# Kernel optimization log

Hardware: AMD Instinct MI355X
Metric: run time of the kernel (lower is better)

The kernel has to match this reference:

```python
import jax, jax.numpy as jnp
import numpy as np

B, S, D, H, HD, L, E, K, M, V = 1, 2048, 1024, 16, 64, 2, 8, 2, 768, 32000
EPS = 1e-06
THETA = 1000000.0


def rmsnorm(x, w, eps=EPS):
    xf = x.astype(jnp.float32)
    var = jnp.mean(xf * xf, axis=-1, keepdims=True)
    return (w * (xf * jax.lax.rsqrt(var + eps))).astype(x.dtype)


def apply_rope(x, cos, sin):
    # x: [B,S,H,HD], cos/sin: [S,HD]; rotate_half convention (HF Qwen3)
    c = cos[None, :, None, :]
    s = sin[None, :, None, :]
    x1, x2 = jnp.split(x, 2, axis=-1)
    rot = jnp.concatenate([-x2, x1], axis=-1)
    return x * c + rot * s


def setup_inputs() -> dict:
    key = jax.random.key(0)
    ks = jax.random.split(key, 16)
    std = 0.02
    inp = {}
    inp['input_ids'] = jax.random.randint(ks[0], (B, S), 0, V)
    inp['embed'] = jax.random.normal(ks[1], (V, D), jnp.float32) * std
    inp['wq'] = jax.random.normal(ks[2], (L, D, H * HD), jnp.float32) * std
    inp['wk'] = jax.random.normal(ks[3], (L, D, H * HD), jnp.float32) * std
    inp['wv'] = jax.random.normal(ks[4], (L, D, H * HD), jnp.float32) * std
    inp['wo'] = jax.random.normal(ks[5], (L, H * HD, D), jnp.float32) * std
    inp['q_norm_w'] = jnp.ones((L, HD), jnp.float32)
    inp['k_norm_w'] = jnp.ones((L, HD), jnp.float32)
    inp['attn_norm_w'] = jnp.ones((L, D), jnp.float32)
    inp['ffn_norm_w'] = jnp.ones((L, D), jnp.float32)
    inp['gate_w'] = jax.random.normal(ks[6], (L, D, E), jnp.float32) * std
    inp['w_gate'] = jax.random.normal(ks[7], (L, E, D, M), jnp.float32) * std
    inp['w_up'] = jax.random.normal(ks[8], (L, E, D, M), jnp.float32) * std
    inp['w_down'] = jax.random.normal(ks[9], (L, E, M, D), jnp.float32) * std
    inp['final_norm_w'] = jnp.ones((D,), jnp.float32)
    inp['out_w'] = jax.random.normal(ks[10], (D, V), jnp.float32) * (D ** -0.5)
    # rope cache: cos/sin with duplicated freqs (HF default rope)
    inv_freq = 1.0 / (THETA ** (jnp.arange(0, HD, 2, dtype=jnp.float32) / HD))
    freqs = jnp.outer(jnp.arange(S, dtype=jnp.float32), inv_freq)  # [S,HD/2]
    emb = jnp.concatenate([freqs, freqs], axis=-1)  # [S,HD]
    inp['cos'] = jnp.cos(emb)
    inp['sin'] = jnp.sin(emb)
    return inp


def reference(input_ids, embed, wq, wk, wv, wo, q_norm_w, k_norm_w, attn_norm_w,
              ffn_norm_w, gate_w, w_gate, w_up, w_down, final_norm_w, out_w, cos, sin):
    h = embed[input_ids]  # [B,S,D]
    causal = jnp.tril(jnp.ones((S, S), bool))[None, None]  # [1,1,S,S]
    scale = 1.0 / np.sqrt(HD)

    def layer(h, p):
        Wq, Wk, Wv, Wo, qn, kn, an, fn, gw, Wg, Wu, Wd = p
        # --- attention ---
        x = rmsnorm(h, an)
        q = (x @ Wq).reshape(B, S, H, HD)
        k = (x @ Wk).reshape(B, S, H, HD)
        v = (x @ Wv).reshape(B, S, H, HD)
        q = apply_rope(rmsnorm(q, qn), cos, sin)
        k = apply_rope(rmsnorm(k, kn), cos, sin)
        scores = jnp.einsum('bqhd,bkhd->bhqk', q, k) * scale
        scores = jnp.where(causal, scores, jnp.finfo(scores.dtype).min)
        attn = jax.nn.softmax(scores, axis=-1)
        o = jnp.einsum('bhqk,bkhd->bqhd', attn, v).reshape(B, S, H * HD) @ Wo
        h = h + o
        # --- sparse MoE ---
        x = rmsnorm(h, fn).reshape(-1, D)  # [T,D]
        probs = jax.nn.softmax((x @ gw).astype(jnp.float32), axis=-1)  # [T,E]
        vals, idx = jax.lax.top_k(probs, K)
        vals = vals / jnp.sum(vals, axis=-1, keepdims=True)  # norm_topk_prob=True
        T = x.shape[0]
        dense = jnp.zeros((T, E), x.dtype).at[jnp.arange(T)[:, None], idx].set(vals.astype(x.dtype))
        g = jnp.einsum('td,edm->tem', x, Wg)
        u = jnp.einsum('td,edm->tem', x, Wu)
        y = jnp.einsum('tem,emd->ted', jax.nn.silu(g) * u, Wd)
        moe = jnp.einsum('te,ted->td', dense, y).reshape(B, S, D)
        return h + moe, None

    h, _ = jax.lax.scan(layer, h, (wq, wk, wv, wo, q_norm_w, k_norm_w, attn_norm_w,
                                   ffn_norm_w, gate_w, w_gate, w_up, w_down))
    h = rmsnorm(h, final_norm_w)
    return h @ out_w  # [B,S,V]
```

## Files before the change

### kernel.cpp

```cpp
#include <hip/hip_runtime.h>
#include <hip/hip_bf16.h>


constexpr int S_ = 2048, D_ = 1024, H_ = 16, HD_ = 64, E_ = 8, MF_ = 768, V_ = 32000;

typedef short  short8 __attribute__((ext_vector_type(8)));
typedef float  f32x4  __attribute__((ext_vector_type(4)));

static __device__ __forceinline__ unsigned short f2bf(float f) {
    unsigned u = __float_as_uint(f);
    u += 0x7FFF + ((u >> 16) & 1);
    return (unsigned short)(u >> 16);
}

__global__ __launch_bounds__(256) void k_gather(const int* __restrict__ ids,
                                                const float* __restrict__ emb,
                                                float* __restrict__ h) {
    int tok = blockIdx.x;
    int id  = ids[tok];
    const float4* src = (const float4*)(emb + (long)id * D_);
    float4*       dst = (float4*)(h + (long)tok * D_);
    dst[threadIdx.x] = src[threadIdx.x];
}

template <int BF>
__global__ __launch_bounds__(256) void k_rmsnorm(const float* __restrict__ in,
                                                 const float* __restrict__ w,
                                                 float* __restrict__ outf,
                                                 unsigned short* __restrict__ outb) {
    int row = blockIdx.x, t = threadIdx.x;
    float4 x = ((const float4*)(in + (long)row * D_))[t];
    float ss = x.x * x.x + x.y * x.y + x.z * x.z + x.w * x.w;
#pragma unroll
    for (int m = 32; m >= 1; m >>= 1) ss += __shfl_xor(ss, m);
    __shared__ float ps[4];
    if ((t & 63) == 0) ps[t >> 6] = ss;
    __syncthreads();
    float tot   = ps[0] + ps[1] + ps[2] + ps[3];
    float scale = 1.0f / sqrtf(tot * (1.0f / D_) + 1e-6f);
    float4 wv = ((const float4*)w)[t];
    float4 o;
    o.x = x.x * scale * wv.x; o.y = x.y * scale * wv.y;
    o.z = x.z * scale * wv.z; o.w = x.w * scale * wv.w;
    if (BF) {
        ushort4 ub;
        ub.x = f2bf(o.x); ub.y = f2bf(o.y); ub.z = f2bf(o.z); ub.w = f2bf(o.w);
        *(ushort4*)(outb + (long)row * D_ + t * 4) = ub;
    } else {
        ((float4*)(outf + (long)row * D_))[t] = o;
    }
}

__global__ __launch_bounds__(256) void k_qkrope(float* __restrict__ q, float* __restrict__ k,
                                                const float* __restrict__ qn,
                                                const float* __restrict__ kn,
                                                const float* __restrict__ cosb,
                                                const float* __restrict__ sinb) {
    int wid  = (blockIdx.x << 2) | (threadIdx.x >> 6);
    int lane = threadIdx.x & 63;
    int tensor = wid >> 15;
    int rem    = wid & 32767;
    int tok = rem >> 4, head = rem & 15;
    float* ptr = tensor ? k : q;
    const float* nw = tensor ? kn : qn;
    long off = ((long)tok * H_ + head) * HD_ + lane;
    float v = ptr[off];
    float ss = v * v;
#pragma unroll
    for (int m = 32; m >= 1; m >>= 1) ss += __shfl_xor(ss, m);
    float xn = v * (1.0f / sqrtf(ss * (1.0f / HD_) + 1e-6f)) * nw[lane];
    float other = __shfl_xor(xn, 32);
    float rot = (lane < 32) ? -other : other;
    ptr[off] = xn * cosb[tok * HD_ + lane] + rot * sinb[tok * HD_ + lane];
}

static __device__ __forceinline__ void splitpack2(float x0, float x1,
                                                  unsigned& wh, unsigned& wm,
                                                  unsigned& wl) {
    unsigned u0 = __float_as_uint(x0), u1 = __float_as_uint(x1);
    unsigned h0 = u0 & 0xFFFF0000u,    h1 = u1 & 0xFFFF0000u;
    float r0 = x0 - __uint_as_float(h0), r1 = x1 - __uint_as_float(h1);
    unsigned m0 = __float_as_uint(r0) & 0xFFFF0000u;
    unsigned m1 = __float_as_uint(r1) & 0xFFFF0000u;
    float s0 = r0 - __uint_as_float(m0), s1 = r1 - __uint_as_float(m1);
    unsigned l0 = __float_as_uint(s0),   l1 = __float_as_uint(s1);
    wh = (h0 >> 16) | h1;
    wm = (m0 >> 16) | m1;
    wl = (l0 >> 16) | (l1 & 0xFFFF0000u);
}

static __device__ __forceinline__ void split8(const float* v,
                                              uint4& qh, uint4& qm, uint4& ql) {
    unsigned ph[4], pm[4], pl[4];
#pragma unroll
    for (int j = 0; j < 4; j++) splitpack2(v[2 * j], v[2 * j + 1], ph[j], pm[j], pl[j]);
    qh = make_uint4(ph[0], ph[1], ph[2], ph[3]);
    qm = make_uint4(pm[0], pm[1], pm[2], pm[3]);
    ql = make_uint4(pl[0], pl[1], pl[2], pl[3]);
}

template <int IND, int EPI>
__global__ __launch_bounds__(256) void k_gemm_s6(const float* __restrict__ A,
                                                 const float* __restrict__ B0,
                                                 const float* __restrict__ B1,
                                                 const float* __restrict__ B2,
                                                 float* __restrict__ C,
                                                 const int* __restrict__ offs,
                                                 const int* __restrict__ rows,
                                                 const float* __restrict__ rwgt,
                                                 float* __restrict__ hout,
                                                 int Mtot, int N, int K,
                                                 long bStrideZ, long cStrideZ) {
    int z = blockIdx.z;
    int ms, me;
    if (offs) { ms = offs[z]; me = offs[z + 1]; }
    else      { ms = 0; me = Mtot; }
    int p0 = ms + blockIdx.y * 128;
    if (p0 >= me) return;
    const float* Bz;
    if (B1) Bz = (z == 0) ? B0 : (z == 1) ? B1 : B2;
    else    Bz = B0 + (long)z * bStrideZ;
    float* Cz = C ? (C + (long)z * cStrideZ) : nullptr;
    int n0 = blockIdx.x * 128;

    __shared__ __align__(16) unsigned short As[3][128][40];
    __shared__ __align__(16) unsigned short Bs[3][128][40];

    int t = threadIdx.x;
    int lane = t & 63, wave = t >> 6;
    int wm = (wave >> 1) * 64, wn = (wave & 1) * 64;
    int ln = lane & 15, lq = lane >> 4;

    f32x4 acc[4][4];
    f32x4 zero4 = {0.f, 0.f, 0.f, 0.f};
#pragma unroll
    for (int r = 0; r < 4; r++)
#pragma unroll
        for (int c = 0; c < 4; c++) acc[r][c] = zero4;

    int arow = t >> 1, ak0 = (t & 1) * 16;
    const float* aptr = nullptr;
    {
        int pA = p0 + arow;
        if (pA < me) {
            int srow = IND ? rows[pA] : pA;
            aptr = A + (long)srow * K + ak0;
        }
    }
    int brow = t >> 1, bk0 = (t & 1) * 16;
    const float* bbase = Bz + (n0 + brow);

    for (int k0 = 0; k0 < K; k0 += 32) {
        float va[16];
        if (aptr) {
#pragma unroll
            for (int c4 = 0; c4 < 4; c4++) {
                float4 f = *(const float4*)(aptr + k0 + c4 * 4);
                va[c4 * 4 + 0] = f.x; va[c4 * 4 + 1] = f.y;
                va[c4 * 4 + 2] = f.z; va[c4 * 4 + 3] = f.w;
            }
        } else {
#pragma unroll
            for (int j = 0; j < 16; j++) va[j] = 0.f;
        }
        uint4 ah0, am0, al0, ah1, am1, al1;
        split8(va,     ah0, am0, al0);
        split8(va + 8, ah1, am1, al1);
        float vb[16];
        {
            const float* bp = bbase + (long)(k0 + bk0) * N;
#pragma unroll
            for (int j = 0; j < 16; j++) vb[j] = bp[(long)j * N];
        }
        uint4 bh0, bm0, bl0, bh1, bm1, bl1;
        split8(vb,     bh0, bm0, bl0);
        split8(vb + 8, bh1, bm1, bl1);

        __syncthreads();
        *(uint4*)&As[0][arow][ak0]     = ah0;
        *(uint4*)&As[0][arow][ak0 + 8] = ah1;
        *(uint4*)&As[1][arow][ak0]     = am0;
        *(uint4*)&As[1][arow][ak0 + 8] = am1;
        *(uint4*)&As[2][arow][ak0]     = al0;
        *(uint4*)&As[2][arow][ak0 + 8] = al1;
        *(uint4*)&Bs[0][brow][bk0]     = bh0;
        *(uint4*)&Bs[0][brow][bk0 + 8] = bh1;
        *(uint4*)&Bs[1][brow][bk0]     = bm0;
        *(uint4*)&Bs[1][brow][bk0 + 8] = bm1;
        *(uint4*)&Bs[2][brow][bk0]     = bl0;
        *(uint4*)&Bs[2][brow][bk0 + 8] = bl1;
        __syncthreads();

        short8 fah[4], fam[4], fal[4];
#pragma unroll
        for (int r = 0; r < 4; r++) {
            fah[r] = *(const short8*)&As[0][wm + 16 * r + ln][lq * 8];
            fam[r] = *(const short8*)&As[1][wm + 16 * r + ln][lq * 8];
            fal[r] = *(const short8*)&As[2][wm + 16 * r + ln][lq * 8];
        }
#pragma unroll
        for (int c = 0; c < 4; c++) {
            short8 fbh = *(const short8*)&Bs[0][wn + 16 * c + ln][lq * 8];
            short8 fbm = *(const short8*)&Bs[1][wn + 16 * c + ln][lq * 8];
            short8 fbl = *(const short8*)&Bs[2][wn + 16 * c + ln][lq * 8];
#pragma unroll
            for (int r = 0; r < 4; r++) {
                f32x4 a2 = acc[r][c];
                a2 = __builtin_amdgcn_mfma_f32_16x16x32_bf16(fah[r], fbh, a2, 0, 0, 0);
                a2 = __builtin_amdgcn_mfma_f32_16x16x32_bf16(fah[r], fbm, a2, 0, 0, 0);
                a2 = __builtin_amdgcn_mfma_f32_16x16x32_bf16(fam[r], fbh, a2, 0, 0, 0);
                a2 = __builtin_amdgcn_mfma_f32_16x16x32_bf16(fah[r], fbl, a2, 0, 0, 0);
                a2 = __builtin_amdgcn_mfma_f32_16x16x32_bf16(fam[r], fbm, a2, 0, 0, 0);
                a2 = __builtin_amdgcn_mfma_f32_16x16x32_bf16(fal[r], fbh, a2, 0, 0, 0);
                acc[r][c] = a2;
            }
        }
    }

#pragma unroll
    for (int r = 0; r < 4; r++)
#pragma unroll
        for (int c = 0; c < 4; c++) {
            int rowb = wm + 16 * r + lq * 4;
            int col  = n0 + wn + 16 * c + ln;
#pragma unroll
            for (int i = 0; i < 4; i++) {
                int p = p0 + rowb + i;
                if (p >= me) continue;
                if (EPI == 2) {
                    atomicAdd(hout + (long)rows[p] * N + col, rwgt[p] * acc[r][c][i]);
                } else if (EPI == 1) {
                    float* cp = Cz + (long)p * N + col;
                    *cp += acc[r][c][i];
                } else {
                    Cz[(long)p * N + col] = acc[r][c][i];
                }
            }
        }
}

__global__ __launch_bounds__(256) void k_attn(const float* __restrict__ q,
                                              const float* __restrict__ k,
                                              const float* __restrict__ v,
                                              float* __restrict__ o) {
    int head = blockIdx.y;
    int q0   = blockIdx.x * 32;
    __shared__ __align__(16) float Qs[32][68];
    __shared__ __align__(16) float Kt[64][68];
    __shared__ __align__(16) float Vs[64][68];
    __shared__ __align__(16) float Ss[32][68];
    __shared__ float red[32][8];
    __shared__ float mrow[32], lrow[32], arow[32];
    int t = threadIdx.x;
    int r = t >> 3, c0 = (t & 7) * 8;
    float o8[8] = {0.f, 0.f, 0.f, 0.f, 0.f, 0.f, 0.f, 0.f};
    {
        int qr = t >> 3, d0 = (t & 7) * 8;
        const float* qp = q + ((long)(q0 + qr) * H_ + head) * HD_ + d0;
        *(float4*)&Qs[qr][d0]     = *(const float4*)qp;
        *(float4*)&Qs[qr][d0 + 4] = *(const float4*)(qp + 4);
    }
    if (t < 32) { mrow[t] = -3.402823466e38f; lrow[t] = 0.f; }
    int ktmax = (q0 + 31) >> 6;
    for (int kt = 0; kt <= ktmax; kt++) {
        __syncthreads();
        {
            int row = t >> 2, d0 = (t & 3) * 16;
            const float* kp = k + ((long)(kt * 64 + row) * H_ + head) * HD_ + d0;
            const float* vp = v + ((long)(kt * 64 + row) * H_ + head) * HD_ + d0;
#pragma unroll
            for (int j = 0; j < 4; j++) {
                float4 kv = *(const float4*)(kp + 4 * j);
                float4 vv = *(const float4*)(vp + 4 * j);
                *(float4*)&Vs[row][d0 + 4 * j] = vv;
                Kt[d0 + 4 * j + 0][row] = kv.x;
                Kt[d0 + 4 * j + 1][row] = kv.y;
                Kt[d0 + 4 * j + 2][row] = kv.z;
                Kt[d0 + 4 * j + 3][row] = kv.w;
            }
        }
        __syncthreads();
        float s8[8] = {0.f, 0.f, 0.f, 0.f, 0.f, 0.f, 0.f, 0.f};
#pragma unroll 8
        for (int d = 0; d < 64; d++) {
            float qv = Qs[r][d];
            float4 ka = *(const float4*)&Kt[d][c0];
            float4 kb = *(const float4*)&Kt[d][c0 + 4];
            s8[0] = fmaf(qv, ka.x, s8[0]); s8[1] = fmaf(qv, ka.y, s8[1]);
            s8[2] = fmaf(qv, ka.z, s8[2]); s8[3] = fmaf(qv, ka.w, s8[3]);
            s8[4] = fmaf(qv, kb.x, s8[4]); s8[5] = fmaf(qv, kb.y, s8[5]);
            s8[6] = fmaf(qv, kb.z, s8[6]); s8[7] = fmaf(qv, kb.w, s8[7]);
        }
        int qrow = q0 + r;
        float mx = -3.402823466e38f;
#pragma unroll
        for (int j = 0; j < 8; j++) {
            int col = kt * 64 + c0 + j;
            s8[j] = (col <= qrow) ? s8[j] * 0.125f : -3.402823466e38f;
            mx = fmaxf(mx, s8[j]);
        }
        red[r][t & 7] = mx;
        __syncthreads();
        if (t < 32) {
            float m0 = mrow[t];
            float mt = red[t][0];
#pragma unroll
            for (int j = 1; j < 8; j++) mt = fmaxf(mt, red[t][j]);
            float mn = fmaxf(m0, mt);
            mrow[t] = mn;
            arow[t] = expf(m0 - mn);
        }
        __syncthreads();
        float mn = mrow[r], al = arow[r];
        float sum = 0.f;
#pragma unroll
        for (int j = 0; j < 8; j++) {
            float e = expf(s8[j] - mn);
            s8[j] = e; sum += e;
        }
        red[r][t & 7] = sum;
        *(float4*)&Ss[r][c0]     = make_float4(s8[0], s8[1], s8[2], s8[3]);
        *(float4*)&Ss[r][c0 + 4] = make_float4(s8[4], s8[5], s8[6], s8[7]);
#pragma unroll
        for (int j = 0; j < 8; j++) o8[j] *= al;
        __syncthreads();
        if (t < 32) {
            float su = red[t][0] + red[t][1] + red[t][2] + red[t][3] +
                       red[t][4] + red[t][5] + red[t][6] + red[t][7];
            lrow[t] = lrow[t] * arow[t] + su;
        }
#pragma unroll 8
        for (int kk2 = 0; kk2 < 64; kk2++) {
            float p = Ss[r][kk2];
            float4 va = *(const float4*)&Vs[kk2][c0];
            float4 vb = *(const float4*)&Vs[kk2][c0 + 4];
            o8[0] = fmaf(p, va.x, o8[0]); o8[1] = fmaf(p, va.y, o8[1]);
            o8[2] = fmaf(p, va.z, o8[2]); o8[3] = fmaf(p, va.w, o8[3]);
            o8[4] = fmaf(p, vb.x, o8[4]); o8[5] = fmaf(p, vb.y, o8[5]);
            o8[6] = fmaf(p, vb.w * 0.f + vb.z, o8[6]); o8[7] = fmaf(p, vb.w, o8[7]);
        }
    }
    __syncthreads();
    float invl = 1.0f / lrow[r];
    float* op = o + ((long)(q0 + r) * H_ + head) * HD_ + c0;
    *(float4*)op       = make_float4(o8[0] * invl, o8[1] * invl, o8[2] * invl, o8[3] * invl);
    *(float4*)(op + 4) = make_float4(o8[4] * invl, o8[5] * invl, o8[6] * invl, o8[7] * invl);
}

__global__ __launch_bounds__(256) void k_router(const float* __restrict__ x,
                                                const float* __restrict__ gw,
                                                int* __restrict__ idx, float* __restrict__ wgt,
                                                int* __restrict__ cnt) {
    int tok  = (blockIdx.x << 2) | (threadIdx.x >> 6);
    int lane = threadIdx.x & 63;
    float acc[8] = {0.f, 0.f, 0.f, 0.f, 0.f, 0.f, 0.f, 0.f};
    for (int i = 0; i < 16; i++) {
        int d = lane + i * 64;
        float xv = x[(long)tok * D_ + d];
        const float* gp = gw + (long)d * E_;
#pragma unroll
        for (int e = 0; e < 8; e++) acc[e] = fmaf(xv, gp[e], acc[e]);
    }
#pragma unroll
    for (int e = 0; e < 8; e++)
#pragma unroll
        for (int m = 32; m >= 1; m >>= 1) acc[e] += __shfl_xor(acc[e], m);
    if (lane == 0) {
        int i1 = 0; float m1 = acc[0];
        for (int e = 1; e < 8; e++) if (acc[e] > m1) { m1 = acc[e]; i1 = e; }
        int i2 = -1; float m2 = -3.402823466e38f;
        for (int e = 0; e < 8; e++) if (e != i1 && acc[e] > m2) { m2 = acc[e]; i2 = e; }
        float w1 = 1.0f / (1.0f + expf(m2 - m1));
        idx[tok * 2] = i1; idx[tok * 2 + 1] = i2;
        wgt[tok * 2] = w1; wgt[tok * 2 + 1] = 1.0f - w1;
        atomicAdd(&cnt[i1], 1);
        atomicAdd(&cnt[i2], 1);
    }
}

__global__ void k_offsets(const int* __restrict__ cnt, int* __restrict__ off) {
    if (threadIdx.x == 0) {
        int run = 0;
        for (int e = 0; e < 8; e++) { off[e] = run; run += cnt[e]; }
        off[8] = run;
    }
}

__global__ __launch_bounds__(256) void k_scatter(const int* __restrict__ idx,
                                                 const float* __restrict__ wgt,
                                                 const int* __restrict__ off,
                                                 int* __restrict__ fill,
                                                 int* __restrict__ rows,
                                                 float* __restrict__ rwgt) {
    int tok = blockIdx.x * 256 + threadIdx.x;
#pragma unroll
    for (int j = 0; j < 2; j++) {
        int e = idx[tok * 2 + j];
        int pos = off[e] + atomicAdd(&fill[e], 1);
        rows[pos] = tok;
        rwgt[pos] = wgt[tok * 2 + j];
    }
}

__global__ __launch_bounds__(256) void k_silumul(const float* __restrict__ g,
                                                 const float* __restrict__ u,
                                                 float* __restrict__ z) {
    long i = (long)(blockIdx.x * 256 + threadIdx.x) * 4;
    float4 gv = *(const float4*)(g + i);
    float4 uv = *(const float4*)(u + i);
    float4 zv;
    zv.x = gv.x / (1.f + expf(-gv.x)) * uv.x;
    zv.y = gv.y / (1.f + expf(-gv.y)) * uv.y;
    zv.z = gv.z / (1.f + expf(-gv.z)) * uv.z;
    zv.w = gv.w / (1.f + expf(-gv.w)) * uv.w;
    *(float4*)(z + i) = zv;
}

__global__ __launch_bounds__(256) void k_transcast(const float* __restrict__ in,
                                                   unsigned short* __restrict__ out) {
    int c0 = blockIdx.x * 32;
    int r0 = blockIdx.y * 32;
    __shared__ __align__(16) float T[32][36];
    int t = threadIdx.x;
    {
        int row = t >> 3, cq = (t & 7) * 4;
        *(float4*)&T[row][cq] = *(const float4*)(in + (long)(r0 + row) * V_ + c0 + cq);
    }
    __syncthreads();
    {
        int n = t >> 3, kq = (t & 7) * 4;
        ushort4 u;
        u.x = f2bf(T[kq + 0][n]); u.y = f2bf(T[kq + 1][n]);
        u.z = f2bf(T[kq + 2][n]); u.w = f2bf(T[kq + 3][n]);
        *(ushort4*)(out + (long)(c0 + n) * D_ + r0 + kq) = u;
    }
}

__global__ __launch_bounds__(256) void k_gemm_bf16(const unsigned short* __restrict__ A,
                                                   const unsigned short* __restrict__ BT,
                                                   float* __restrict__ C) {
    int m0 = blockIdx.x * 128, n0 = blockIdx.y * 128;
    __shared__ __align__(16) unsigned short As[128][40];
    __shared__ __align__(16) unsigned short Bs[128][40];
    int t = threadIdx.x;
    int lane = t & 63, wave = t >> 6;
    int wm = (wave >> 1) * 64, wn = (wave & 1) * 64;
    int ln = lane & 15, lq = lane >> 4;
    f32x4 acc[4][4];
    f32x4 zero4 = {0.f, 0.f, 0.f, 0.f};
#pragma unroll
    for (int r = 0; r < 4; r++)
#pragma unroll
        for (int c = 0; c < 4; c++) acc[r][c] = zero4;
    int rowA = t >> 1;
    int q1 = (t * 2) & 3, q2 = (t * 2 + 1) & 3;
    for (int k0 = 0; k0 < 1024; k0 += 32) {
        const uint4* ap = (const uint4*)(A + (long)(m0 + rowA) * 1024 + k0);
        const uint4* bp = (const uint4*)(BT + (long)(n0 + rowA) * 1024 + k0);
        uint4 a0 = ap[q1], a1 = ap[q2];
        uint4 b0 = bp[q1], b1 = bp[q2];
        __syncthreads();
        *(uint4*)&As[rowA][q1 * 8] = a0;
        *(uint4*)&As[rowA][q2 * 8] = a1;
        *(uint4*)&Bs[rowA][q1 * 8] = b0;
        *(uint4*)&Bs[rowA][q2 * 8] = b1;
        __syncthreads();
        short8 a[4], b[4];
#pragma unroll
        for (int r = 0; r < 4; r++) a[r] = *(const short8*)&As[wm + 16 * r + ln][lq * 8];
#pragma unroll
        for (int c = 0; c < 4; c++) b[c] = *(const short8*)&Bs[wn + 16 * c + ln][lq * 8];
#pragma unroll
        for (int r = 0; r < 4; r++)
#pragma unroll
            for (int c = 0; c < 4; c++)
                acc[r][c] = __builtin_amdgcn_mfma_f32_16x16x32_bf16(a[r], b[c], acc[r][c], 0, 0, 0);
    }
#pragma unroll
    for (int r = 0; r < 4; r++)
#pragma unroll
        for (int c = 0; c < 4; c++) {
            int row = m0 + wm + 16 * r + lq * 4;
            int col = n0 + wn + 16 * c + ln;
#pragma unroll
            for (int i = 0; i < 4; i++)
                C[(long)(row + i) * V_ + col] = acc[r][c][i];
        }
}

extern "C" void kernel_launch(void* const* d_in, const int* in_sizes, int n_in,
                              void* d_out, int out_size, void* d_ws, size_t ws_size,
                              hipStream_t stream) {
    (void)in_sizes; (void)n_in; (void)out_size; (void)ws_size;
    const int*   ids   = (const int*)d_in[0];
    const float* embed = (const float*)d_in[1];
    const float* wq    = (const float*)d_in[2];
    const float* wk    = (const float*)d_in[3];
    const float* wv    = (const float*)d_in[4];
    const float* wo    = (const float*)d_in[5];
    const float* qnw   = (const float*)d_in[6];
    const float* knw   = (const float*)d_in[7];
    const float* anw   = (const float*)d_in[8];
    const float* fnw   = (const float*)d_in[9];
    const float* gatew = (const float*)d_in[10];
    const float* wgate = (const float*)d_in[11];
    const float* wup   = (const float*)d_in[12];
    const float* wdown = (const float*)d_in[13];
    const float* finw  = (const float*)d_in[14];
    const float* outw  = (const float*)d_in[15];
    const float* cosb  = (const float*)d_in[16];
    const float* sinb  = (const float*)d_in[17];
    float* out = (float*)d_out;

    char* w = (char*)d_ws;
    float* h  = (float*)(w);
    float* x  = (float*)(w + 8388608);
    float* q  = (float*)(w + 16777216);
    float* kk = (float*)(w + 25165824);
    float* vv = (float*)(w + 33554432);
    float* ao = (float*)(w + 41943040);
    float* g  = (float*)(w + 50331648);
    float* u  = (float*)(w + 62914560);
    float* z  = (float*)(w + 75497472);
    unsigned short* hn  = (unsigned short*)(w + 88080384);
    unsigned short* owT = (unsigned short*)(w + 16777216);
    char* rbase = w + 92274688;
    int*   idx  = (int*)(rbase);
    float* wgt  = (float*)(rbase + 16384);
    int*   cnt  = (int*)(rbase + 32768);
    int*   fill = (int*)(rbase + 32768 + 32);
    int*   offs = (int*)(rbase + 32768 + 64);
    int*   rows = (int*)(rbase + 32768 + 128);
    float* rwgt = (float*)(rbase + 32768 + 128 + 16384);

    k_gather<<<2048, 256, 0, stream>>>(ids, embed, h);

    for (int l = 0; l < 2; l++) {
        const float* wq_l = wq + (long)l * D_ * D_;
        const float* wk_l = wk + (long)l * D_ * D_;
        const float* wv_l = wv + (long)l * D_ * D_;
        const float* wo_l = wo + (long)l * D_ * D_;
        const float* an_l = anw + l * D_;
        const float* fn_l = fnw + l * D_;
        const float* qn_l = qnw + l * HD_;
        const float* kn_l = knw + l * HD_;
        const float* gw_l = gatew + (long)l * D_ * E_;
        const float* wg_l = wgate + (long)l * E_ * D_ * MF_;
        const float* wu_l = wup   + (long)l * E_ * D_ * MF_;
        const float* wd_l = wdown + (long)l * E_ * MF_ * D_;

        k_rmsnorm<0><<<2048, 256, 0, stream>>>(h, an_l, x, nullptr);
        k_gemm_s6<0, 0><<<dim3(8, 16, 3), 256, 0, stream>>>(x, wq_l, wk_l, wv_l, q,
            nullptr, nullptr, nullptr, nullptr, 2048, 1024, 1024, 0, 2048L * 1024);
        k_qkrope<<<16384, 256, 0, stream>>>(q, kk, qn_l, kn_l, cosb, sinb);
        k_attn<<<dim3(64, 16), 256, 0, stream>>>(q, kk, vv, ao);
        k_gemm_s6<0, 1><<<dim3(8, 16, 1), 256, 0, stream>>>(ao, wo_l, nullptr, nullptr, h,
            nullptr, nullptr, nullptr, nullptr, 2048, 1024, 1024, 0, 0);
        k_rmsnorm<0><<<2048, 256, 0, stream>>>(h, fn_l, x, nullptr);
        hipMemsetAsync(cnt, 0, 64, stream);
        k_router<<<512, 256, 0, stream>>>(x, gw_l, idx, wgt, cnt);
        k_offsets<<<1, 64, 0, stream>>>(cnt, offs);
        k_scatter<<<8, 256, 0, stream>>>(idx, wgt, offs, fill, rows, rwgt);
        k_gemm_s6<1, 0><<<dim3(6, 16, 8), 256, 0, stream>>>(x, wg_l, nullptr, nullptr, g,
            offs, rows, nullptr, nullptr, 4096, 768, 1024, (long)D_ * MF_, 0);
        k_gemm_s6<1, 0><<<dim3(6, 16, 8), 256, 0, stream>>>(x, wu_l, nullptr, nullptr, u,
            offs, rows, nullptr, nullptr, 4096, 768, 1024, (long)D_ * MF_, 0);
        k_silumul<<<3072, 256, 0, stream>>>(g, u, z);
        k_gemm_s6<0, 2><<<dim3(8, 16, 8), 256, 0, stream>>>(z, wd_l, nullptr, nullptr, nullptr,
            offs, rows, rwgt, h, 4096, 1024, 768, (long)MF_ * D_, 0);
    }

    k_rmsnorm<1><<<2048, 256, 0, stream>>>(h, finw, nullptr, hn);
    k_transcast<<<dim3(1000, 32), 256, 0, stream>>>(outw, owT);
    k_gemm_bf16<<<dim3(16, 250), 256, 0, stream>>>(hn, owT, out);
}
```

Before: 2.500 ms.

## Rewrite causal attention to use bf16x3 split MFMA with 64-row query tiles

Replaces the scalar FP32 flash-attention kernel with one that splits Q, K, V and P into three bf16 components and runs both QK^T and PV on 16x16x32 bf16 MFMA, using six products to keep roughly FP32 accuracy. Query tiles grow from 32 to 64 rows, each wave owns 16 rows, and softmax reductions use cross-lane shuffles instead of shared-memory reductions and extra barriers. Half the heads walk query tiles in reverse order to balance the causal workload across the grid. The cost is extra conversion work and more LDS traffic for the split operands and the transposed V staging.

```diff
diff --git a/kernel.cpp b/kernel.cpp
--- a/kernel.cpp
+++ b/kernel.cpp
@@ -11,6 +11,10 @@
     unsigned u = __float_as_uint(f);
     u += 0x7FFF + ((u >> 16) & 1);
     return (unsigned short)(u >> 16);
+}
+
+static __device__ __forceinline__ short8 u2s8(uint4 u) {
+    union { uint4 a; short8 b; } x; x.a = u; return x.b;
 }
 
 __global__ __launch_bounds__(256) void k_gather(const int* __restrict__ ids,
@@ -239,112 +243,178 @@
         }
 }
 
-__global__ __launch_bounds__(256) void k_attn(const float* __restrict__ q,
-                                              const float* __restrict__ k,
-                                              const float* __restrict__ v,
-                                              float* __restrict__ o) {
+__global__ __launch_bounds__(256) void k_attn_mfma(const float* __restrict__ q,
+                                                   const float* __restrict__ k,
+                                                   const float* __restrict__ v,
+                                                   float* __restrict__ o) {
     int head = blockIdx.y;
-    int q0   = blockIdx.x * 32;
-    __shared__ __align__(16) float Qs[32][68];
-    __shared__ __align__(16) float Kt[64][68];
-    __shared__ __align__(16) float Vs[64][68];
-    __shared__ __align__(16) float Ss[32][68];
-    __shared__ float red[32][8];
-    __shared__ float mrow[32], lrow[32], arow[32];
+    int qi = ((blockIdx.y >> 3) & 1) ? (int)(gridDim.x - 1 - blockIdx.x) : (int)blockIdx.x;
+    int q0 = qi * 64;
+
+    __shared__ __align__(16) unsigned short Ks[3][64][72];
+    __shared__ __align__(16) unsigned short Vt[3][64][72];
+    __shared__ __align__(16) float Ps[64][68];
+
     int t = threadIdx.x;
-    int r = t >> 3, c0 = (t & 7) * 8;
-    float o8[8] = {0.f, 0.f, 0.f, 0.f, 0.f, 0.f, 0.f, 0.f};
+    int lane = t & 63, w = t >> 6;
+    int ln = lane & 15, lq = lane >> 4;
+
+    short8 qh[2], qm[2], qlr[2];
     {
-        int qr = t >> 3, d0 = (t & 7) * 8;
-        const float* qp = q + ((long)(q0 + qr) * H_ + head) * HD_ + d0;
-        *(float4*)&Qs[qr][d0]     = *(const float4*)qp;
-        *(float4*)&Qs[qr][d0 + 4] = *(const float4*)(qp + 4);
-    }
-    if (t < 32) { mrow[t] = -3.402823466e38f; lrow[t] = 0.f; }
-    int ktmax = (q0 + 31) >> 6;
-    for (int kt = 0; kt <= ktmax; kt++) {
+        const float* qp = q + ((long)(q0 + 16 * w + ln) * H_ + head) * HD_;
+#pragma unroll
+        for (int ks = 0; ks < 2; ks++) {
+            float vq[8];
+            float4 f0 = *(const float4*)(qp + 32 * ks + lq * 8);
+            float4 f1 = *(const float4*)(qp + 32 * ks + lq * 8 + 4);
+            vq[0] = f0.x; vq[1] = f0.y; vq[2] = f0.z; vq[3] = f0.w;
+            vq[4] = f1.x; vq[5] = f1.y; vq[6] = f1.z; vq[7] = f1.w;
+            uint4 hh, mm, ll;
+            split8(vq, hh, mm, ll);
+            qh[ks] = u2s8(hh); qm[ks] = u2s8(mm); qlr[ks] = u2s8(ll);
+        }
+    }
+
+    f32x4 oc[4];
+    f32x4 zero4 = {0.f, 0.f, 0.f, 0.f};
+#pragma unroll
+    for (int c = 0; c < 4; c++) oc[c] = zero4;
+    float m_run[4], l_run[4];
+#pragma unroll
+    for (int i = 0; i < 4; i++) { m_run[i] = -3.402823466e38f; l_run[i] = 0.f; }
+
+    for (int kt = 0; kt <= qi; kt++) {
         __syncthreads();
         {
-            int row = t >> 2, d0 = (t & 3) * 16;
-            const float* kp = k + ((long)(kt * 64 + row) * H_ + head) * HD_ + d0;
-            const float* vp = v + ((long)(kt * 64 + row) * H_ + head) * HD_ + d0;
+            int kr = t >> 2, kq4 = (t & 3) * 16;
+            const float* kp = k + ((long)(kt * 64 + kr) * H_ + head) * HD_ + kq4;
+            float vk[16];
 #pragma unroll
             for (int j = 0; j < 4; j++) {
-                float4 kv = *(const float4*)(kp + 4 * j);
-                float4 vv = *(const float4*)(vp + 4 * j);
-                *(float4*)&Vs[row][d0 + 4 * j] = vv;
-                Kt[d0 + 4 * j + 0][row] = kv.x;
-                Kt[d0 + 4 * j + 1][row] = kv.y;
-                Kt[d0 + 4 * j + 2][row] = kv.z;
-                Kt[d0 + 4 * j + 3][row] = kv.w;
+                float4 f = *(const float4*)(kp + 4 * j);
+                vk[4 * j + 0] = f.x; vk[4 * j + 1] = f.y;
+                vk[4 * j + 2] = f.z; vk[4 * j + 3] = f.w;
+            }
+            uint4 h0, m0, l0, h1, m1, l1;
+            split8(vk,     h0, m0, l0);
+            split8(vk + 8, h1, m1, l1);
+            *(uint4*)&Ks[0][kr][kq4]     = h0; *(uint4*)&Ks[0][kr][kq4 + 8] = h1;
+            *(uint4*)&Ks[1][kr][kq4]     = m0; *(uint4*)&Ks[1][kr][kq4 + 8] = m1;
+            *(uint4*)&Ks[2][kr][kq4]     = l0; *(uint4*)&Ks[2][kr][kq4 + 8] = l1;
+            const float* vp = v + ((long)(kt * 64 + lane) * H_ + head) * HD_ + w * 16;
+            float vvv[16];
+#pragma unroll
+            for (int j = 0; j < 4; j++) {
+                float4 f = *(const float4*)(vp + 4 * j);
+                vvv[4 * j + 0] = f.x; vvv[4 * j + 1] = f.y;
+                vvv[4 * j + 2] = f.z; vvv[4 * j + 3] = f.w;
+            }
+#pragma unroll
+            for (int j = 0; j < 16; j++) {
+                float x = vvv[j];
+                unsigned uu = __float_as_uint(x);
+                unsigned hh = uu & 0xFFFF0000u;
+                float rr = x - __uint_as_float(hh);
+                unsigned mm2 = __float_as_uint(rr) & 0xFFFF0000u;
+                float ss2 = rr - __uint_as_float(mm2);
+                Vt[0][w * 16 + j][lane] = (unsigned short)(hh >> 16);
+                Vt[1][w * 16 + j][lane] = (unsigned short)(mm2 >> 16);
+                Vt[2][w * 16 + j][lane] = (unsigned short)(__float_as_uint(ss2) >> 16);
             }
         }
         __syncthreads();
-        float s8[8] = {0.f, 0.f, 0.f, 0.f, 0.f, 0.f, 0.f, 0.f};
-#pragma unroll 8
-        for (int d = 0; d < 64; d++) {
-            float qv = Qs[r][d];
-            float4 ka = *(const float4*)&Kt[d][c0];
-            float4 kb = *(const float4*)&Kt[d][c0 + 4];
-            s8[0] = fmaf(qv, ka.x, s8[0]); s8[1] = fmaf(qv, ka.y, s8[1]);
-            s8[2] = fmaf(qv, ka.z, s8[2]); s8[3] = fmaf(qv, ka.w, s8[3]);
-            s8[4] = fmaf(qv, kb.x, s8[4]); s8[5] = fmaf(qv, kb.y, s8[5]);
-            s8[6] = fmaf(qv, kb.z, s8[6]); s8[7] = fmaf(qv, kb.w, s8[7]);
-        }
-        int qrow = q0 + r;
-        float mx = -3.402823466e38f;
-#pragma unroll
-        for (int j = 0; j < 8; j++) {
-            int col = kt * 64 + c0 + j;
-            s8[j] = (col <= qrow) ? s8[j] * 0.125f : -3.402823466e38f;
-            mx = fmaxf(mx, s8[j]);
-        }
-        red[r][t & 7] = mx;
-        __syncthreads();
-        if (t < 32) {
-            float m0 = mrow[t];
-            float mt = red[t][0];
-#pragma unroll
-            for (int j = 1; j < 8; j++) mt = fmaxf(mt, red[t][j]);
-            float mn = fmaxf(m0, mt);
-            mrow[t] = mn;
-            arow[t] = expf(m0 - mn);
-        }
-        __syncthreads();
-        float mn = mrow[r], al = arow[r];
-        float sum = 0.f;
-#pragma unroll
-        for (int j = 0; j < 8; j++) {
-            float e = expf(s8[j] - mn);
-            s8[j] = e; sum += e;
-        }
-        red[r][t & 7] = sum;
-        *(float4*)&Ss[r][c0]     = make_float4(s8[0], s8[1], s8[2], s8[3]);
-        *(float4*)&Ss[r][c0 + 4] = make_float4(s8[4], s8[5], s8[6], s8[7]);
-#pragma unroll
-        for (int j = 0; j < 8; j++) o8[j] *= al;
-        __syncthreads();
-        if (t < 32) {
-            float su = red[t][0] + red[t][1] + red[t][2] + red[t][3] +
-                       red[t][4] + red[t][5] + red[t][6] + red[t][7];
-            lrow[t] = lrow[t] * arow[t] + su;
-        }
-#pragma unroll 8
-        for (int kk2 = 0; kk2 < 64; kk2++) {
-            float p = Ss[r][kk2];
-            float4 va = *(const float4*)&Vs[kk2][c0];
-            float4 vb = *(const float4*)&Vs[kk2][c0 + 4];
-            o8[0] = fmaf(p, va.x, o8[0]); o8[1] = fmaf(p, va.y, o8[1]);
-            o8[2] = fmaf(p, va.z, o8[2]); o8[3] = fmaf(p, va.w, o8[3]);
-            o8[4] = fmaf(p, vb.x, o8[4]); o8[5] = fmaf(p, vb.y, o8[5]);
-            o8[6] = fmaf(p, vb.w * 0.f + vb.z, o8[6]); o8[7] = fmaf(p, vb.w, o8[7]);
-        }
-    }
-    __syncthreads();
-    float invl = 1.0f / lrow[r];
-    float* op = o + ((long)(q0 + r) * H_ + head) * HD_ + c0;
-    *(float4*)op       = make_float4(o8[0] * invl, o8[1] * invl, o8[2] * invl, o8[3] * invl);
-    *(float4*)(op + 4) = make_float4(o8[4] * invl, o8[5] * invl, o8[6] * invl, o8[7] * invl);
+
+        f32x4 sc[4];
+#pragma unroll
+        for (int c = 0; c < 4; c++) sc[c] = zero4;
+#pragma unroll
+        for (int ks = 0; ks < 2; ks++) {
+#pragma unroll
+            for (int c = 0; c < 4; c++) {
+                const int co = 16 * c + ln, ko = 32 * ks + lq * 8;
+                short8 bh = *(const short8*)&Ks[0][co][ko];
+                short8 bm = *(const short8*)&Ks[1][co][ko];
+                short8 bl = *(const short8*)&Ks[2][co][ko];
+                f32x4 a2 = sc[c];
+                a2 = __builtin_amdgcn_mfma_f32_16x16x32_bf16(qh[ks],  bh, a2, 0, 0, 0);
+                a2 = __builtin_amdgcn_mfma_f32_16x16x32_bf16(qh[ks],  bm, a2, 0, 0, 0);
+                a2 = __builtin_amdgcn_mfma_f32_16x16x32_bf16(qm[ks],  bh, a2, 0, 0, 0);
+                a2 = __builtin_amdgcn_mfma_f32_16x16x32_bf16(qh[ks],  bl, a2, 0, 0, 0);
+                a2 = __builtin_amdgcn_mfma_f32_16x16x32_bf16(qm[ks],  bm, a2, 0, 0, 0);
+                a2 = __builtin_amdgcn_mfma_f32_16x16x32_bf16(qlr[ks], bh, a2, 0, 0, 0);
+                sc[c] = a2;
+            }
+        }
+
+#pragma unroll
+        for (int i = 0; i < 4; i++) {
+            int qg = q0 + 16 * w + 4 * lq + i;
+            float mx = -3.402823466e38f;
+#pragma unroll
+            for (int c = 0; c < 4; c++) {
+                int kvg = kt * 64 + 16 * c + ln;
+                float s = sc[c][i] * 0.125f;
+                s = (kvg <= qg) ? s : -3.402823466e38f;
+                sc[c][i] = s;
+                mx = fmaxf(mx, s);
+            }
+            mx = fmaxf(mx, __shfl_xor(mx, 1));
+            mx = fmaxf(mx, __shfl_xor(mx, 2));
+            mx = fmaxf(mx, __shfl_xor(mx, 4));
+            mx = fmaxf(mx, __shfl_xor(mx, 8));
+            float mn = fmaxf(m_run[i], mx);
+            float al = expf(m_run[i] - mn);
+            m_run[i] = mn;
+            float sum = 0.f;
+#pragma unroll
+            for (int c = 0; c < 4; c++) {
+                float e = expf(sc[c][i] - mn);
+                Ps[16 * w + 4 * lq + i][16 * c + ln] = e;
+                sum += e;
+            }
+            sum += __shfl_xor(sum, 1);
+            sum += __shfl_xor(sum, 2);
+            sum += __shfl_xor(sum, 4);
+            sum += __shfl_xor(sum, 8);
+            l_run[i] = l_run[i] * al + sum;
+#pragma unroll
+            for (int c = 0; c < 4; c++) oc[c][i] *= al;
+        }
+
+#pragma unroll
+        for (int ks = 0; ks < 2; ks++) {
+            float pv8[8];
+            *(float4*)&pv8[0] = *(const float4*)&Ps[16 * w + ln][32 * ks + lq * 8];
+            *(float4*)&pv8[4] = *(const float4*)&Ps[16 * w + ln][32 * ks + lq * 8 + 4];
+            uint4 ph4, pm4, pl4;
+            split8(pv8, ph4, pm4, pl4);
+            short8 pah = u2s8(ph4), pam = u2s8(pm4), pal = u2s8(pl4);
+#pragma unroll
+            for (int c = 0; c < 4; c++) {
+                const int co = 16 * c + ln, ko = 32 * ks + lq * 8;
+                short8 bh = *(const short8*)&Vt[0][co][ko];
+                short8 bm = *(const short8*)&Vt[1][co][ko];
+                short8 bl = *(const short8*)&Vt[2][co][ko];
+                f32x4 a2 = oc[c];
+                a2 = __builtin_amdgcn_mfma_f32_16x16x32_bf16(pah, bh, a2, 0, 0, 0);
+                a2 = __builtin_amdgcn_mfma_f32_16x16x32_bf16(pah, bm, a2, 0, 0, 0);
+                a2 = __builtin_amdgcn_mfma_f32_16x16x32_bf16(pam, bh, a2, 0, 0, 0);
+                a2 = __builtin_amdgcn_mfma_f32_16x16x32_bf16(pah, bl, a2, 0, 0, 0);
+                a2 = __builtin_amdgcn_mfma_f32_16x16x32_bf16(pam, bm, a2, 0, 0, 0);
+                a2 = __builtin_amdgcn_mfma_f32_16x16x32_bf16(pal, bh, a2, 0, 0, 0);
+                oc[c] = a2;
+            }
+        }
+    }
+
+#pragma unroll
+    for (int i = 0; i < 4; i++) {
+        float invl = 1.0f / l_run[i];
+        int qg = q0 + 16 * w + 4 * lq + i;
+        float* op = o + ((long)qg * H_ + head) * HD_;
+#pragma unroll
+        for (int c = 0; c < 4; c++) op[16 * c + ln] = oc[c][i] * invl;
+    }
 }
 
 __global__ __launch_bounds__(256) void k_router(const float* __restrict__ x,
@@ -553,7 +623,7 @@
         k_gemm_s6<0, 0><<<dim3(8, 16, 3), 256, 0, stream>>>(x, wq_l, wk_l, wv_l, q,
             nullptr, nullptr, nullptr, nullptr, 2048, 1024, 1024, 0, 2048L * 1024);
         k_qkrope<<<16384, 256, 0, stream>>>(q, kk, qn_l, kn_l, cosb, sinb);
-        k_attn<<<dim3(64, 16), 256, 0, stream>>>(q, kk, vv, ao);
+        k_attn_mfma<<<dim3(32, 16), 256, 0, stream>>>(q, kk, vv, ao);
         k_gemm_s6<0, 1><<<dim3(8, 16, 1), 256, 0, stream>>>(ao, wo_l, nullptr, nullptr, h,
             nullptr, nullptr, nullptr, nullptr, 2048, 1024, 1024, 0, 0);
         k_rmsnorm<0><<<2048, 256, 0, stream>>>(h, fn_l, x, nullptr);
```

After: 2.131 ms. -14.8%, faster.
